# Optimization experiments

Hardware: AMD Instinct MI355X
Metric: run time of the kernel (lower is better)

## Reference

```python
import jax, jax.numpy as jnp
import numpy as np

N = 8192
FIN = 128
FOUT = 64
NEG_BIG = -9e15


def setup_inputs() -> dict:
    key = jax.random.key(0)
    k1, k2, k3, k4 = jax.random.split(key, 4)
    x = jax.random.normal(k1, (N, FIN), dtype=jnp.float32)
    adj = jax.random.randint(k2, (N, N), 0, 2, dtype=jnp.int32)
    stdv_w = 1.0 / np.sqrt(FOUT)
    W = jax.random.uniform(k3, (FIN, FOUT), dtype=jnp.float32, minval=-stdv_w, maxval=stdv_w)
    # weight2: stdv = 1/sqrt(1) = 1
    a = jax.random.uniform(k4, (2 * FOUT, 1), dtype=jnp.float32, minval=-1.0, maxval=1.0)
    return {"x": x, "adj": adj, "W": W, "a": a}


def reference(x, adj, W, a):
    # h = x W  -> [N, Fout]
    h = x @ W
    # e_ij = relu(a^T [h_i || h_j]) decomposed exactly: a1.h_i + a2.h_j
    a1 = a[:FOUT, 0]  # [Fout]
    a2 = a[FOUT:, 0]  # [Fout]
    s1 = h @ a1  # [N]
    s2 = h @ a2  # [N]
    e = jax.nn.relu(s1[:, None] + s2[None, :])  # [N, N]
    att_logits = jnp.where(adj > 0, e, jnp.float32(NEG_BIG))
    attention = jax.nn.softmax(att_logits, axis=-1)  # [N, N]
    # dropout omitted (eval mode / p applied only in training)
    out = attention @ h  # [N, Fout]
    return out[None]  # [1, N, Fout] matching batch_size=1 reshape
```

## Files before the change

kernel.cpp:

```cpp
#include <hip/hip_runtime.h>
#include <cstdint>
#include <cstddef>

#define NN 8192
#define FIN 128
#define FOUT 64
#define BM 32
#define BN 64
#define JSPLIT 8
#define JCH (NN / JSPLIT)
#define NCHUNK (JCH / BN)
#define LDP 72

typedef __bf16 bf16x8 __attribute__((ext_vector_type(8)));
typedef unsigned short u16x8 __attribute__((ext_vector_type(8)));
typedef float f32x4 __attribute__((ext_vector_type(4)));

__device__ __forceinline__ unsigned short f2bf(float f) {
    unsigned u = __float_as_uint(f);
    u += 0x7FFFu + ((u >> 16) & 1u);
    return (unsigned short)(u >> 16);
}
__device__ __forceinline__ float bf2f(unsigned short b) {
    return __uint_as_float(((unsigned)b) << 16);
}

__global__ __launch_bounds__(256) void gat_prep(
    const float* __restrict__ x, const float* __restrict__ W,
    const float* __restrict__ a, float* __restrict__ s1,
    float* __restrict__ s2, unsigned short* __restrict__ Ht,
    unsigned int* __restrict__ s2max_enc)
{
    __shared__ __align__(16) float Wt[FOUT][FIN + 4];
    __shared__ float wa1[FIN], wa2[FIN];
    __shared__ float ash[2 * FOUT];
    __shared__ float s2sh[BM];

    const int tid = threadIdx.x;
    const int i0 = blockIdx.x * BM;

    for (int it = 0; it < 32; ++it) {
        int idx = it * 256 + tid;
        int k = idx >> 6, t = idx & 63;
        Wt[t][k] = W[idx];
    }
    if (tid < 2 * FOUT) ash[tid] = a[tid];
    __syncthreads();

    if (tid < FIN) {
        int k = tid;
        float acc = 0.f;
        #pragma unroll 8
        for (int t = 0; t < FOUT; ++t) acc = fmaf(Wt[t][k], ash[t], acc);
        wa1[k] = acc;
    } else {
        int k = tid - FIN;
        float acc = 0.f;
        #pragma unroll 8
        for (int t = 0; t < FOUT; ++t) acc = fmaf(Wt[t][k], ash[FOUT + t], acc);
        wa2[k] = acc;
    }
    __syncthreads();

    {
        int r = tid >> 3;
        int seg = tid & 7;
        const float* xp = x + (size_t)(i0 + r) * FIN + seg * 16;
        float d1 = 0.f, d2 = 0.f;
        #pragma unroll
        for (int m = 0; m < 16; ++m) {
            float xv = xp[m];
            d1 = fmaf(xv, wa1[seg * 16 + m], d1);
            d2 = fmaf(xv, wa2[seg * 16 + m], d2);
        }
        #pragma unroll
        for (int mk = 1; mk < 8; mk <<= 1) {
            d1 += __shfl_xor(d1, mk);
            d2 += __shfl_xor(d2, mk);
        }
        if (seg == 0) {
            s1[i0 + r] = d1;
            s2[i0 + r] = d2;
            s2sh[r] = d2;
        }
    }

    {
        const int lane = tid & 63;
        const int wv = tid >> 6;
        const int ih = wv & 1, nh = wv >> 1;
        const int m = lane & 15, quad = lane >> 4;
        f32x4 hacc0 = {0.f, 0.f, 0.f, 0.f};
        f32x4 hacc1 = {0.f, 0.f, 0.f, 0.f};
        const float* xrow = x + (size_t)(i0 + ih * 16 + m) * FIN + quad * 8;
        #pragma unroll
        for (int ks = 0; ks < 4; ++ks) {
            const float* xp = xrow + ks * 32;
            u16x8 ua;
            #pragma unroll
            for (int jj = 0; jj < 8; ++jj) ua[jj] = f2bf(xp[jj]);
            bf16x8 af = __builtin_bit_cast(bf16x8, ua);
            {
                const float* wp = &Wt[nh * 32 + m][ks * 32 + quad * 8];
                u16x8 ub;
                #pragma unroll
                for (int jj = 0; jj < 8; ++jj) ub[jj] = f2bf(wp[jj]);
                bf16x8 bfr = __builtin_bit_cast(bf16x8, ub);
                hacc0 = __builtin_amdgcn_mfma_f32_16x16x32_bf16(af, bfr, hacc0, 0, 0, 0);
            }
            {
                const float* wp = &Wt[nh * 32 + 16 + m][ks * 32 + quad * 8];
                u16x8 ub;
                #pragma unroll
                for (int jj = 0; jj < 8; ++jj) ub[jj] = f2bf(wp[jj]);
                bf16x8 bfr = __builtin_bit_cast(bf16x8, ub);
                hacc1 = __builtin_amdgcn_mfma_f32_16x16x32_bf16(af, bfr, hacc1, 0, 0, 0);
            }
        }
        #pragma unroll
        for (int reg = 0; reg < 4; ++reg) {
            int irow = i0 + ih * 16 + quad * 4 + reg;
            int t0 = nh * 32 + m;
            Ht[(size_t)t0 * NN + irow] = f2bf(hacc0[reg]);
            Ht[(size_t)(t0 + 16) * NN + irow] = f2bf(hacc1[reg]);
        }
    }
    __syncthreads();
    if (tid == 0) {
        float mx = s2sh[0];
        #pragma unroll
        for (int r = 1; r < BM; ++r) mx = fmaxf(mx, s2sh[r]);
        unsigned ub = __float_as_uint(mx);
        unsigned enc = (ub & 0x80000000u) ? ~ub : (ub | 0x80000000u);
        atomicMax(s2max_enc, enc);
    }
}

__global__ __launch_bounds__(256, 6) void gat_attn(
    const int* __restrict__ adj, const float* __restrict__ s1,
    const float* __restrict__ s2, const unsigned short* __restrict__ Ht,
    const unsigned int* __restrict__ s2max_enc,
    float* __restrict__ pacc, float* __restrict__ pl)
{
    __shared__ __align__(16) unsigned short p_lds[2][BM][LDP];
    __shared__ __align__(16) float s2sh[JCH];
    __shared__ float s1v[BM], Mv[BM];

    const int tid = threadIdx.x;
    const int bx = blockIdx.x;
    const int r = bx >> 3;
    const int js = bx & 7;
    const int i0 = r * BM;
    const int j0 = js * JCH;

    const int li = tid >> 4;
    const int jg = (tid & 15) * 4;

    const int* adjp0 = adj + (size_t)(i0 + li) * NN + j0 + jg;
    const int* adjp1 = adjp0 + 16 * NN;

    int4 ca0 = *(const int4*)adjp0;
    int4 ca1 = *(const int4*)adjp1;

    const int lane = tid & 63;
    const int wv = tid >> 6;
    const int ih = wv & 1, nh = wv >> 1;
    const int cm = lane & 15, quad = lane >> 4;

    const unsigned short* htb0 = Ht + (size_t)(nh * 32 + cm) * NN + j0 + quad * 8;
    const unsigned short* htb1 = htb0 + (size_t)16 * NN;

    {
        int idx = tid * 4;
        *(float4*)&s2sh[idx] = *(const float4*)(s2 + j0 + idx);
        unsigned u = *s2max_enc;
        float S2MAX = (u & 0x80000000u) ? __uint_as_float(u ^ 0x80000000u)
                                        : __uint_as_float(~u);
        if (tid < BM) {
            float s = s1[i0 + tid];
            s1v[tid] = s;
            Mv[tid] = fmaxf(0.f, s + S2MAX);
        }
    }
    __syncthreads();

    f32x4 acc0 = {0.f, 0.f, 0.f, 0.f};
    f32x4 acc1 = {0.f, 0.f, 0.f, 0.f};
    float psA = 0.f, psB = 0.f;

    const float s1a = s1v[li], Ma = Mv[li];
    const float s1b = s1v[li + 16], Mb = Mv[li + 16];

    for (int c = 0; c < NCHUNK; ++c) {
        const int buf = c & 1;

        bf16x8 b00 = *(const bf16x8*)(htb0 + c * BN);
        bf16x8 b01 = *(const bf16x8*)(htb1 + c * BN);
        bf16x8 b10 = *(const bf16x8*)(htb0 + c * BN + 32);
        bf16x8 b11 = *(const bf16x8*)(htb1 + c * BN + 32);

        const int cn = (c + 1 < NCHUNK) ? (c + 1) : c;
        int4 na0 = *(const int4*)(adjp0 + cn * BN);
        int4 na1 = *(const int4*)(adjp1 + cn * BN);

        {
            const int* av0 = (const int*)&ca0;
            const int* av1 = (const int*)&ca1;
            const float* s2v = &s2sh[c * BN + jg];
            unsigned short qa[4], qb[4];
            #pragma unroll
            for (int jj = 0; jj < 4; ++jj) {
                float s2x = s2v[jj];
                float eA = fmaxf(s1a + s2x, 0.f);
                float pA = (av0[jj] > 0) ? __expf(eA - Ma) : 0.f;
                qa[jj] = f2bf(pA);
                psA += bf2f(qa[jj]);
                float eB = fmaxf(s1b + s2x, 0.f);
                float pB = (av1[jj] > 0) ? __expf(eB - Mb) : 0.f;
                qb[jj] = f2bf(pB);
                psB += bf2f(qb[jj]);
            }
            *(ushort4*)&p_lds[buf][li][jg]      = make_ushort4(qa[0], qa[1], qa[2], qa[3]);
            *(ushort4*)&p_lds[buf][li + 16][jg] = make_ushort4(qb[0], qb[1], qb[2], qb[3]);
        }

        __syncthreads();

        {
            bf16x8 af0 = *(const bf16x8*)&p_lds[buf][ih * 16 + cm][quad * 8];
            bf16x8 af1 = *(const bf16x8*)&p_lds[buf][ih * 16 + cm][32 + quad * 8];
            acc0 = __builtin_amdgcn_mfma_f32_16x16x32_bf16(af0, b00, acc0, 0, 0, 0);
            acc1 = __builtin_amdgcn_mfma_f32_16x16x32_bf16(af0, b01, acc1, 0, 0, 0);
            acc0 = __builtin_amdgcn_mfma_f32_16x16x32_bf16(af1, b10, acc0, 0, 0, 0);
            acc1 = __builtin_amdgcn_mfma_f32_16x16x32_bf16(af1, b11, acc1, 0, 0, 0);
        }

        ca0 = na0; ca1 = na1;
    }

    #pragma unroll
    for (int mk = 1; mk < 16; mk <<= 1) {
        psA += __shfl_xor(psA, mk);
        psB += __shfl_xor(psB, mk);
    }
    if ((tid & 15) == 0) {
        pl[(size_t)js * NN + i0 + li]      = psA;
        pl[(size_t)js * NN + i0 + li + 16] = psB;
    }

    #pragma unroll
    for (int reg = 0; reg < 4; ++reg) {
        int irow = i0 + ih * 16 + quad * 4 + reg;
        int n0 = nh * 32 + cm;
        pacc[((size_t)js * NN + irow) * FOUT + n0]      = acc0[reg];
        pacc[((size_t)js * NN + irow) * FOUT + n0 + 16] = acc1[reg];
    }
}

__global__ __launch_bounds__(256) void gat_combine(
    const float* __restrict__ pacc, const float* __restrict__ pl,
    float* __restrict__ out)
{
    int idx = blockIdx.x * 256 + threadIdx.x;
    int i = idx >> 6;
    float s = 0.f, l = 0.f;
    #pragma unroll
    for (int js = 0; js < JSPLIT; ++js) {
        s += pacc[(size_t)js * NN * FOUT + idx];
        l += pl[(size_t)js * NN + i];
    }
    out[idx] = s / l;
}

extern "C" void kernel_launch(void* const* d_in, const int* in_sizes, int n_in,
                              void* d_out, int out_size, void* d_ws, size_t ws_size,
                              hipStream_t stream) {
    const float* x   = (const float*)d_in[0];
    const int*   adj = (const int*)d_in[1];
    const float* W   = (const float*)d_in[2];
    const float* a   = (const float*)d_in[3];
    float* out = (float*)d_out;

    char* ws = (char*)d_ws;
    float* s1             = (float*)(ws);
    float* s2             = (float*)(ws + 32768);
    unsigned int* s2enc   = (unsigned int*)(ws + 65536);
    unsigned short* Ht    = (unsigned short*)(ws + 66560);
    float* pacc           = (float*)(ws + 66560 + 1048576);
    float* pl             = (float*)(ws + 66560 + 1048576 + 16777216);

    hipMemsetAsync(s2enc, 0, 4, stream);
    gat_prep<<<NN / BM, 256, 0, stream>>>(x, W, a, s1, s2, Ht, s2enc);
    gat_attn<<<(NN / BM) * JSPLIT, 256, 0, stream>>>(adj, s1, s2, Ht, s2enc, pacc, pl);
    gat_combine<<<NN * FOUT / 256, 256, 0, stream>>>(pacc, pl, out);
}
```

Baseline: 402.1 us.

## Drop split-K partials and combine kernel; each block handles full row span

```diff
diff --git a/kernel.cpp b/kernel.cpp
--- a/kernel.cpp
+++ b/kernel.cpp
@@ -5,12 +5,12 @@
 #define NN 8192
 #define FIN 128
 #define FOUT 64
-#define BM 32
+#define BM 16
 #define BN 64
-#define JSPLIT 8
-#define JCH (NN / JSPLIT)
-#define NCHUNK (JCH / BN)
+#define NCHUNK (NN / BN)
 #define LDP 72
+#define PBM 32
+#define NPREP (NN / PBM)
 
 typedef __bf16 bf16x8 __attribute__((ext_vector_type(8)));
 typedef unsigned short u16x8 __attribute__((ext_vector_type(8)));
@@ -29,15 +29,15 @@
     const float* __restrict__ x, const float* __restrict__ W,
     const float* __restrict__ a, float* __restrict__ s1,
     float* __restrict__ s2, unsigned short* __restrict__ Ht,
-    unsigned int* __restrict__ s2max_enc)
+    float* __restrict__ pbmax)
 {
     __shared__ __align__(16) float Wt[FOUT][FIN + 4];
     __shared__ float wa1[FIN], wa2[FIN];
     __shared__ float ash[2 * FOUT];
-    __shared__ float s2sh[BM];
+    __shared__ float s2sh[PBM];
 
     const int tid = threadIdx.x;
-    const int i0 = blockIdx.x * BM;
+    const int i0 = blockIdx.x * PBM;
 
     for (int it = 0; it < 32; ++it) {
         int idx = it * 256 + tid;
@@ -129,147 +129,106 @@
     if (tid == 0) {
         float mx = s2sh[0];
         #pragma unroll
-        for (int r = 1; r < BM; ++r) mx = fmaxf(mx, s2sh[r]);
-        unsigned ub = __float_as_uint(mx);
-        unsigned enc = (ub & 0x80000000u) ? ~ub : (ub | 0x80000000u);
-        atomicMax(s2max_enc, enc);
-    }
-}
-
-__global__ __launch_bounds__(256, 6) void gat_attn(
+        for (int r = 1; r < PBM; ++r) mx = fmaxf(mx, s2sh[r]);
+        pbmax[blockIdx.x] = mx;
+    }
+}
+
+__global__ __launch_bounds__(256, 2) void gat_attn(
     const int* __restrict__ adj, const float* __restrict__ s1,
     const float* __restrict__ s2, const unsigned short* __restrict__ Ht,
-    const unsigned int* __restrict__ s2max_enc,
-    float* __restrict__ pacc, float* __restrict__ pl)
+    const float* __restrict__ pbmax, float* __restrict__ out)
 {
     __shared__ __align__(16) unsigned short p_lds[2][BM][LDP];
-    __shared__ __align__(16) float s2sh[JCH];
-    __shared__ float s1v[BM], Mv[BM];
+    __shared__ __align__(16) float s2sh[NN];
+    __shared__ float s1v[BM], lsum[BM];
+    __shared__ float s2m;
 
     const int tid = threadIdx.x;
-    const int bx = blockIdx.x;
-    const int r = bx >> 3;
-    const int js = bx & 7;
-    const int i0 = r * BM;
-    const int j0 = js * JCH;
+    const int i0 = blockIdx.x * BM;
 
     const int li = tid >> 4;
     const int jg = (tid & 15) * 4;
 
-    const int* adjp0 = adj + (size_t)(i0 + li) * NN + j0 + jg;
-    const int* adjp1 = adjp0 + 16 * NN;
-
-    int4 ca0 = *(const int4*)adjp0;
-    int4 ca1 = *(const int4*)adjp1;
+    const int* adjp = adj + (size_t)(i0 + li) * NN + jg;
+    int4 ca = *(const int4*)adjp;
 
     const int lane = tid & 63;
     const int wv = tid >> 6;
-    const int ih = wv & 1, nh = wv >> 1;
     const int cm = lane & 15, quad = lane >> 4;
 
-    const unsigned short* htb0 = Ht + (size_t)(nh * 32 + cm) * NN + j0 + quad * 8;
-    const unsigned short* htb1 = htb0 + (size_t)16 * NN;
-
-    {
-        int idx = tid * 4;
-        *(float4*)&s2sh[idx] = *(const float4*)(s2 + j0 + idx);
-        unsigned u = *s2max_enc;
-        float S2MAX = (u & 0x80000000u) ? __uint_as_float(u ^ 0x80000000u)
-                                        : __uint_as_float(~u);
-        if (tid < BM) {
-            float s = s1[i0 + tid];
-            s1v[tid] = s;
-            Mv[tid] = fmaxf(0.f, s + S2MAX);
-        }
-    }
-    __syncthreads();
-
-    f32x4 acc0 = {0.f, 0.f, 0.f, 0.f};
-    f32x4 acc1 = {0.f, 0.f, 0.f, 0.f};
-    float psA = 0.f, psB = 0.f;
-
-    const float s1a = s1v[li], Ma = Mv[li];
-    const float s1b = s1v[li + 16], Mb = Mv[li + 16];
-
+    const unsigned short* htb = Ht + (size_t)(wv * 16 + cm) * NN + quad * 8;
+
+    #pragma unroll
+    for (int it = 0; it < 8; ++it) {
+        int idx = (it * 256 + tid) * 4;
+        *(float4*)&s2sh[idx] = *(const float4*)(s2 + idx);
+    }
+    if (tid < 64) {
+        float v = pbmax[tid];
+        v = fmaxf(v, pbmax[tid + 64]);
+        v = fmaxf(v, pbmax[tid + 128]);
+        v = fmaxf(v, pbmax[tid + 192]);
+        #pragma unroll
+        for (int mk = 1; mk < 64; mk <<= 1) v = fmaxf(v, __shfl_xor(v, mk));
+        if (tid == 0) s2m = v;
+    }
+    if (tid < BM) s1v[tid] = s1[i0 + tid];
+    __syncthreads();
+
+    const float S2MAX = s2m;
+    const float s1a = s1v[li];
+    const float Ma = fmaxf(0.f, s1a + S2MAX);
+
+    f32x4 acc = {0.f, 0.f, 0.f, 0.f};
+    float ps = 0.f;
+
+    #pragma unroll 2
     for (int c = 0; c < NCHUNK; ++c) {
         const int buf = c & 1;
 
-        bf16x8 b00 = *(const bf16x8*)(htb0 + c * BN);
-        bf16x8 b01 = *(const bf16x8*)(htb1 + c * BN);
-        bf16x8 b10 = *(const bf16x8*)(htb0 + c * BN + 32);
-        bf16x8 b11 = *(const bf16x8*)(htb1 + c * BN + 32);
+        bf16x8 b0 = *(const bf16x8*)(htb + c * BN);
+        bf16x8 b1 = *(const bf16x8*)(htb + c * BN + 32);
 
         const int cn = (c + 1 < NCHUNK) ? (c + 1) : c;
-        int4 na0 = *(const int4*)(adjp0 + cn * BN);
-        int4 na1 = *(const int4*)(adjp1 + cn * BN);
+        int4 na = *(const int4*)(adjp + cn * BN);
 
         {
-            const int* av0 = (const int*)&ca0;
-            const int* av1 = (const int*)&ca1;
+            const int* av = (const int*)&ca;
             const float* s2v = &s2sh[c * BN + jg];
-            unsigned short qa[4], qb[4];
+            unsigned short q[4];
             #pragma unroll
             for (int jj = 0; jj < 4; ++jj) {
-                float s2x = s2v[jj];
-                float eA = fmaxf(s1a + s2x, 0.f);
-                float pA = (av0[jj] > 0) ? __expf(eA - Ma) : 0.f;
-                qa[jj] = f2bf(pA);
-                psA += bf2f(qa[jj]);
-                float eB = fmaxf(s1b + s2x, 0.f);
-                float pB = (av1[jj] > 0) ? __expf(eB - Mb) : 0.f;
-                qb[jj] = f2bf(pB);
-                psB += bf2f(qb[jj]);
+                float e = fmaxf(s1a + s2v[jj], 0.f);
+                float p = (av[jj] > 0) ? __expf(e - Ma) : 0.f;
+                q[jj] = f2bf(p);
+                ps += bf2f(q[jj]);
             }
-            *(ushort4*)&p_lds[buf][li][jg]      = make_ushort4(qa[0], qa[1], qa[2], qa[3]);
-            *(ushort4*)&p_lds[buf][li + 16][jg] = make_ushort4(qb[0], qb[1], qb[2], qb[3]);
+            *(ushort4*)&p_lds[buf][li][jg] = make_ushort4(q[0], q[1], q[2], q[3]);
         }
 
         __syncthreads();
 
         {
-            bf16x8 af0 = *(const bf16x8*)&p_lds[buf][ih * 16 + cm][quad * 8];
-            bf16x8 af1 = *(const bf16x8*)&p_lds[buf][ih * 16 + cm][32 + quad * 8];
-            acc0 = __builtin_amdgcn_mfma_f32_16x16x32_bf16(af0, b00, acc0, 0, 0, 0);
-            acc1 = __builtin_amdgcn_mfma_f32_16x16x32_bf16(af0, b01, acc1, 0, 0, 0);
-            acc0 = __builtin_amdgcn_mfma_f32_16x16x32_bf16(af1, b10, acc0, 0, 0, 0);
-            acc1 = __builtin_amdgcn_mfma_f32_16x16x32_bf16(af1, b11, acc1, 0, 0, 0);
-        }
-
-        ca0 = na0; ca1 = na1;
+            bf16x8 af0 = *(const bf16x8*)&p_lds[buf][cm][quad * 8];
+            bf16x8 af1 = *(const bf16x8*)&p_lds[buf][cm][32 + quad * 8];
+            acc = __builtin_amdgcn_mfma_f32_16x16x32_bf16(af0, b0, acc, 0, 0, 0);
+            acc = __builtin_amdgcn_mfma_f32_16x16x32_bf16(af1, b1, acc, 0, 0, 0);
+        }
+
+        ca = na;
     }
 
     #pragma unroll
-    for (int mk = 1; mk < 16; mk <<= 1) {
-        psA += __shfl_xor(psA, mk);
-        psB += __shfl_xor(psB, mk);
-    }
-    if ((tid & 15) == 0) {
-        pl[(size_t)js * NN + i0 + li]      = psA;
-        pl[(size_t)js * NN + i0 + li + 16] = psB;
-    }
+    for (int mk = 1; mk < 16; mk <<= 1) ps += __shfl_xor(ps, mk);
+    if ((tid & 15) == 0) lsum[li] = ps;
+    __syncthreads();
 
     #pragma unroll
     for (int reg = 0; reg < 4; ++reg) {
-        int irow = i0 + ih * 16 + quad * 4 + reg;
-        int n0 = nh * 32 + cm;
-        pacc[((size_t)js * NN + irow) * FOUT + n0]      = acc0[reg];
-        pacc[((size_t)js * NN + irow) * FOUT + n0 + 16] = acc1[reg];
-    }
-}
-
-__global__ __launch_bounds__(256) void gat_combine(
-    const float* __restrict__ pacc, const float* __restrict__ pl,
-    float* __restrict__ out)
-{
-    int idx = blockIdx.x * 256 + threadIdx.x;
-    int i = idx >> 6;
-    float s = 0.f, l = 0.f;
-    #pragma unroll
-    for (int js = 0; js < JSPLIT; ++js) {
-        s += pacc[(size_t)js * NN * FOUT + idx];
-        l += pl[(size_t)js * NN + i];
-    }
-    out[idx] = s / l;
+        int row = quad * 4 + reg;
+        out[(size_t)(i0 + row) * FOUT + wv * 16 + cm] = acc[reg] / lsum[row];
+    }
 }
 
 extern "C" void kernel_launch(void* const* d_in, const int* in_sizes, int n_in,
@@ -282,15 +241,11 @@
     float* out = (float*)d_out;
 
     char* ws = (char*)d_ws;
-    float* s1             = (float*)(ws);
-    float* s2             = (float*)(ws + 32768);
-    unsigned int* s2enc   = (unsigned int*)(ws + 65536);
-    unsigned short* Ht    = (unsigned short*)(ws + 66560);
-    float* pacc           = (float*)(ws + 66560 + 1048576);
-    float* pl             = (float*)(ws + 66560 + 1048576 + 16777216);
-
-    hipMemsetAsync(s2enc, 0, 4, stream);
-    gat_prep<<<NN / BM, 256, 0, stream>>>(x, W, a, s1, s2, Ht, s2enc);
-    gat_attn<<<(NN / BM) * JSPLIT, 256, 0, stream>>>(adj, s1, s2, Ht, s2enc, pacc, pl);
-    gat_combine<<<NN * FOUT / 256, 256, 0, stream>>>(pacc, pl, out);
-}
+    float* s1          = (float*)(ws);
+    float* s2          = (float*)(ws + 32768);
+    float* pbmax       = (float*)(ws + 65536);
+    unsigned short* Ht = (unsigned short*)(ws + 66560);
+
+    gat_prep<<<NPREP, 256, 0, stream>>>(x, W, a, s1, s2, Ht, pbmax);
+    gat_attn<<<NN / BM, 256, 0, stream>>>(adj, s1, s2, Ht, pbmax, out);
+}
```

Measured after the change: 403.7 us. Within noise of the previous version (+0.4%).
